# Kernel tuning notes

Measured on AMD Instinct MI355X. Metric: run time of the kernel, lower is better.

The kernel has to match this reference:

```python
import jax, jax.numpy as jnp
import numpy as np


def setup_inputs() -> dict:
    key = jax.random.key(0)
    ks = jax.random.split(key, 7)
    b, t, c = 2, 2048, 1024
    s = 0.02  # keep pre-softmax logits in a sane range
    return {
        "query": jax.random.normal(ks[0], (b, t, c), jnp.float32),
        "key": jax.random.normal(ks[1], (b, t, c), jnp.float32),
        "value": jax.random.normal(ks[2], (b, t, c), jnp.float32),
        "in_proj_w": jax.random.normal(ks[3], (3 * c, c), jnp.float32) * s,
        "in_proj_b": jax.random.normal(ks[4], (3 * c,), jnp.float32) * s,
        "out_proj_w": jax.random.normal(ks[5], (c, c), jnp.float32) * s,
        "out_proj_b": jax.random.normal(ks[6], (c,), jnp.float32) * s,
        "window_size": 128,
    }


def reference(query, key, value, in_proj_w, in_proj_b, out_proj_w, out_proj_b, window_size):
    num_heads = 16
    b, t, c = query.shape
    hd = c // num_heads
    wq, wk, wv = in_proj_w[:c], in_proj_w[c:2 * c], in_proj_w[2 * c:]
    bq, bk, bv = in_proj_b[:c], in_proj_b[c:2 * c], in_proj_b[2 * c:]
    # project and split heads: [b, h, t, hd]
    q = (query @ wq.T + bq).reshape(b, t, num_heads, hd).transpose(0, 2, 1, 3)
    k = (key @ wk.T + bk).reshape(b, t, num_heads, hd).transpose(0, 2, 1, 3)
    v = (value @ wv.T + bv).reshape(b, t, num_heads, hd).transpose(0, 2, 1, 3)
    # NOTE: torch adds a *float* attn_mask to the logits. The original mask is
    # 1.0 inside the sliding window, 0.0 outside -- an additive +1 bias, NOT -inf.
    idx = jnp.arange(t)
    band = (jnp.abs(idx[:, None] - idx[None, :]) <= window_size).astype(q.dtype)  # [t, t]
    scale = 1.0 / jnp.sqrt(jnp.asarray(hd, q.dtype))
    logits = jnp.einsum("bhqd,bhkd->bhqk", q * scale, k) + band  # [b,h,t,t]
    attn = jax.nn.softmax(logits, axis=-1)
    out = jnp.einsum("bhqk,bhkd->bhqd", attn, v)  # [b,h,t,hd]
    out = out.transpose(0, 2, 1, 3).reshape(b, t, c)
    return out @ out_proj_w.T + out_proj_b
```

## Files before the change

### kernel.cpp

```cpp
#include <hip/hip_runtime.h>

typedef __attribute__((ext_vector_type(8)))  short short8;
typedef __attribute__((ext_vector_type(4)))  short sh4;
typedef __attribute__((ext_vector_type(4)))  float f32x4;
typedef __attribute__((ext_vector_type(16))) float f32x16;

constexpr int B  = 2;
constexpr int T  = 2048;
constexpr int C  = 1024;
constexpr int H  = 16;
constexpr int HD = 64;

__device__ inline unsigned bf16rne(float a){
  unsigned u = __builtin_bit_cast(unsigned, a);
  u += 0x7fffu + ((u >> 16) & 1u);
  return u >> 16;
}
__device__ inline unsigned bf16pair(float a, float b){
  unsigned ua = __builtin_bit_cast(unsigned, a); ua += 0x7fffu + ((ua >> 16) & 1u);
  unsigned ub = __builtin_bit_cast(unsigned, b); ub += 0x7fffu + ((ub >> 16) & 1u);
  return (ua >> 16) | (ub & 0xffff0000u);
}
__device__ inline void gll16(const void* g, void* l){
  __builtin_amdgcn_global_load_lds(
      (const __attribute__((address_space(1))) unsigned*)g,
      (__attribute__((address_space(3))) unsigned*)l, 16, 0, 0);
}
__device__ inline float exp2f_(float x){
#if __has_builtin(__builtin_amdgcn_exp2f)
  return __builtin_amdgcn_exp2f(x);
#else
  return __builtin_exp2f(x);
#endif
}

__global__ void convert_k(const float* __restrict__ ipw, const float* __restrict__ opw,
                          const float* __restrict__ q, const float* __restrict__ k,
                          const float* __restrict__ v, unsigned* __restrict__ dst)
{
  const int i = blockIdx.x * 256 + threadIdx.x;
  const long e = (long)i * 4;
  const float* src; long off;
  if      (e <  3145728) { src = ipw; off = e; }
  else if (e <  4194304) { src = opw; off = e - 3145728; }
  else if (e <  8388608) { src = q;   off = e - 4194304; }
  else if (e < 12582912) { src = k;   off = e - 8388608; }
  else                   { src = v;   off = e - 12582912; }
  const float4 x = *(const float4*)(src + off);
  dst[i*2+0] = bf16pair(x.x, x.y);
  dst[i*2+1] = bf16pair(x.z, x.w);
}

template<int MODE>
__global__ __launch_bounds__(256, 2) void gemm_k(
    const unsigned short* __restrict__ A0, const unsigned short* __restrict__ A1,
    const unsigned short* __restrict__ A2,
    const unsigned short* __restrict__ Wb, const float* __restrict__ bias,
    unsigned short* __restrict__ Qb, unsigned short* __restrict__ Kb,
    unsigned short* __restrict__ Vt, float* __restrict__ outF)
{
  __shared__ __align__(16) unsigned short As[128*32];
  __shared__ __align__(16) unsigned short Bs[128*32];
  const int tid  = threadIdx.x, lane = tid & 63, wv = tid >> 6;
  const int wm   = wv & 1, wn = wv >> 1;
  const int bm   = blockIdx.x, bn = blockIdx.y;
  const int m16  = lane & 15, quad = lane >> 4;

  const int which = (MODE == 0) ? (bn >> 3) : 0;
  const unsigned short* A = (which == 0) ? A0 : (which == 1 ? A1 : A2);

  f32x4 acc[4][4];
#pragma unroll
  for (int i = 0; i < 4; i++)
#pragma unroll
    for (int j = 0; j < 4; j++) acc[i][j] = (f32x4){0.f, 0.f, 0.f, 0.f};

  const int srow = wv * 32 + (lane >> 2);
  const int skp  = (lane & 3) * 8;

  for (int k0 = 0; k0 < 1024; k0 += 32) {
    __syncthreads();
#pragma unroll
    for (int p = 0; p < 2; p++) {
      gll16(A  + (size_t)(bm*128 + srow + p*16)*1024 + k0 + skp,
            (char*)As + wv*2048 + p*1024);
      gll16(Wb + (size_t)(bn*128 + srow + p*16)*1024 + k0 + skp,
            (char*)Bs + wv*2048 + p*1024);
    }
    __syncthreads();

    short8 af[4], bf[4];
#pragma unroll
    for (int i = 0; i < 4; i++)
      af[i] = *(const short8*)((const char*)As + (wm*64 + i*16 + m16)*64 + quad*16);
#pragma unroll
    for (int j = 0; j < 4; j++)
      bf[j] = *(const short8*)((const char*)Bs + (wn*64 + j*16 + m16)*64 + quad*16);
#pragma unroll
    for (int i = 0; i < 4; i++)
#pragma unroll
      for (int j = 0; j < 4; j++)
        acc[i][j] = __builtin_amdgcn_mfma_f32_16x16x32_bf16(af[i], bf[j], acc[i][j], 0,0,0);
  }

#pragma unroll
  for (int j = 0; j < 4; j++) {
    const int n_e = bn*128 + wn*64 + j*16 + m16;
    const float bj = bias[n_e];
    const int rem = n_e & 1023;
    const int hh = rem >> 6, dd = rem & 63;
#pragma unroll
    for (int i = 0; i < 4; i++) {
      const int mbase = bm*128 + wm*64 + i*16 + quad*4;
      if constexpr (MODE == 1) {
#pragma unroll
        for (int r = 0; r < 4; r++)
          outF[(size_t)(mbase + r) * 1024 + n_e] = acc[i][j][r] + bj;
      } else {
        const int b = mbase >> 11, tl = mbase & 2047;
        if (which == 2) {
          sh4 pv;
#pragma unroll
          for (int r = 0; r < 4; r++) pv[r] = (short)bf16rne(acc[i][j][r] + bj);
          *(sh4*)(Vt + ((size_t)((b*16 + hh)*64 + dd))*2048 + tl) = pv;
        } else {
          unsigned short* dst = (which == 0 ? Qb : Kb);
#pragma unroll
          for (int r = 0; r < 4; r++)
            dst[(size_t)((b*16 + hh)*2048 + tl + r)*64 + dd] =
                (unsigned short)bf16rne(acc[i][j][r] + bj);
        }
      }
    }
  }
}

__global__ __launch_bounds__(256, 2) void attn_k(
    const unsigned short* __restrict__ Qb, const unsigned short* __restrict__ Kb,
    const unsigned short* __restrict__ Vt, const int* __restrict__ wptr,
    unsigned short* __restrict__ ctx)
{
  __shared__ __align__(16) char smem[16896];
  unsigned short* Kl = (unsigned short*)smem;
  unsigned short* Vl = (unsigned short*)(smem + 8192);
  float* Om   = (float*)smem;
  float* lbuf = (float*)(smem + 16384);

  const int tid = threadIdx.x, lane = tid & 63, wv = tid >> 6;
  const int wq = wv >> 1, wk = wv & 1;
  const int h = lane >> 5, ln = lane & 31;
  const bool hs = (h == 1);
  const int qt = blockIdx.x, bh = blockIdx.y;
  const int win = *wptr;
  const int q0 = qt * 64 + wq * 32;
  const size_t hb = (size_t)bh * T * HD;

  constexpr float LOG2E = 1.44269504f;
  constexpr float C1    = 0.125f * LOG2E;

  short8 qf[4];
#pragma unroll
  for (int s = 0; s < 4; s++)
    qf[s] = *(const short8*)(Qb + hb + (size_t)(q0 + ln)*64 + s*16 + h*8);

  short8 onesv;
#pragma unroll
  for (int jj = 0; jj < 8; jj++) onesv[jj] = (short)0x3F80;

  f32x16 O0, O1, Lacc, Zv;
#pragma unroll
  for (int r = 0; r < 16; r++) { O0[r] = 0.f; O1[r] = 0.f; Lacc[r] = 0.f; Zv[r] = 0.f; }
  const int tq = q0 + ln;

  for (int kt = 0; kt < 32; ++kt) {
    __syncthreads();
#pragma unroll
    for (int p = 0; p < 2; p++) {
      const int c2 = wv*2 + p;
      gll16(Kb + hb + (size_t)(kt*64 + lane)*64 + c2*8, (char*)Kl + c2*1024);
      gll16(Vt + hb + (size_t)lane*T + kt*64 + c2*8,    (char*)Vl + c2*1024);
    }
    __syncthreads();

    f32x16 st;
#pragma unroll
    for (int s = 0; s < 4; s++) {
      const short8 kf = *(const short8*)((const char*)Kl + (2*s + h)*1024 + (wk*32 + ln)*16);
      st = __builtin_amdgcn_mfma_f32_32x32x16_bf16(kf, qf[s], (s == 0 ? Zv : st), 0, 0, 0);
    }

    const int kb = kt*64 + wk*32;
    int sep = 0;
    if (kb > q0 + 31) sep = kb - (q0 + 31);
    else if (q0 > kb + 31) sep = q0 - (kb + 31);
    const int d1 = kb + 31 - q0, d2 = q0 + 31 - kb;
    const int dmax = max(d1 < 0 ? -d1 : d1, d2 < 0 ? -d2 : d2);

    float pr[16];
    if (sep > win) {
#pragma unroll
      for (int r = 0; r < 16; r++) pr[r] = exp2f_(st[r] * C1);
    } else if (dmax <= win) {
#pragma unroll
      for (int r = 0; r < 16; r++) pr[r] = exp2f_(__builtin_fmaf(st[r], C1, LOG2E));
    } else {
      const int tkb = kb + 4*h;
#pragma unroll
      for (int r = 0; r < 16; r++) {
        const int tk = tkb + (r & 3) + 8*(r >> 2);
        int dd = tq - tk; dd = dd < 0 ? -dd : dd;
        pr[r] = exp2f_(__builtin_fmaf(st[r], C1, dd <= win ? LOG2E : 0.0f));
      }
    }

    unsigned pk[8];
#pragma unroll
    for (int g = 0; g < 8; g++)
      pk[g] = __builtin_amdgcn_perm(__builtin_bit_cast(unsigned, pr[2*g+1]),
                                    __builtin_bit_cast(unsigned, pr[2*g]),
                                    0x07060302u);

#pragma unroll
    for (int c = 0; c < 2; c++) {
      const unsigned sh0 = (unsigned)__shfl_xor((int)pk[4*c+0], 32, 64);
      const unsigned sh1 = (unsigned)__shfl_xor((int)pk[4*c+1], 32, 64);
      const unsigned sh2 = (unsigned)__shfl_xor((int)pk[4*c+2], 32, 64);
      const unsigned sh3 = (unsigned)__shfl_xor((int)pk[4*c+3], 32, 64);
      union { unsigned u[4]; short8 v; } P;
      P.u[0] = hs ? sh2 : pk[4*c+0];
      P.u[1] = hs ? sh3 : pk[4*c+1];
      P.u[2] = hs ? pk[4*c+2] : sh0;
      P.u[3] = hs ? pk[4*c+3] : sh1;
#pragma unroll
      for (int dt = 0; dt < 2; dt++) {
        const short8 vf = *(const short8*)((const char*)Vl + (wk*4 + 2*c + h)*1024 + (dt*32 + ln)*16);
        if (dt == 0) O0 = __builtin_amdgcn_mfma_f32_32x32x16_bf16(P.v, vf, O0, 0,0,0);
        else         O1 = __builtin_amdgcn_mfma_f32_32x32x16_bf16(P.v, vf, O1, 0,0,0);
      }
      Lacc = __builtin_amdgcn_mfma_f32_32x32x16_bf16(P.v, onesv, Lacc, 0,0,0);
    }
  }

  __syncthreads();
  if (wk == 1) {
#pragma unroll
    for (int r = 0; r < 16; r++) {
      Om[wq*2048 + r*64 + lane]        = O0[r];
      Om[wq*2048 + (16 + r)*64 + lane] = O1[r];
    }
    if (ln == 0) {
#pragma unroll
      for (int r = 0; r < 16; r++)
        lbuf[wq*32 + (r & 3) + 8*(r >> 2) + 4*h] = Lacc[r];
    }
  }
  __syncthreads();
  if (wk == 0) {
    const int b = bh >> 4, hh = bh & 15;
#pragma unroll
    for (int r = 0; r < 16; r++) {
      const int qrow = (r & 3) + 8*(r >> 2) + 4*h;
      const float lt = Lacc[r] + lbuf[wq*32 + qrow];
      const float linv = 1.0f / lt;
      const int t = q0 + qrow;
      const float o0 = (O0[r] + Om[wq*2048 + r*64 + lane]) * linv;
      const float o1 = (O1[r] + Om[wq*2048 + (16 + r)*64 + lane]) * linv;
      unsigned short* cp = ctx + (size_t)(b*2048 + t)*1024 + hh*64;
      cp[ln]      = (unsigned short)bf16rne(o0);
      cp[32 + ln] = (unsigned short)bf16rne(o1);
    }
  }
}

extern "C" void kernel_launch(void* const* d_in, const int* in_sizes, int n_in,
                              void* d_out, int out_size, void* d_ws, size_t ws_size,
                              hipStream_t stream)
{
  const float* query = (const float*)d_in[0];
  const float* key   = (const float*)d_in[1];
  const float* value = (const float*)d_in[2];
  const float* ipw   = (const float*)d_in[3];
  const float* ipb   = (const float*)d_in[4];
  const float* opw   = (const float*)d_in[5];
  const float* opb   = (const float*)d_in[6];
  const int*   win   = (const int*)d_in[7];

  char* ws = (char*)d_ws;
  unsigned short* Winbf  = (unsigned short*)(ws);
  unsigned short* Woutbf = (unsigned short*)(ws + 6291456);
  unsigned short* Qin    = (unsigned short*)(ws + 8388608);
  unsigned short* Kin    = (unsigned short*)(ws + 16777216);
  unsigned short* Vin    = (unsigned short*)(ws + 25165824);
  unsigned short* Qb     = (unsigned short*)(ws + 33554432);
  unsigned short* Kb     = (unsigned short*)(ws + 41943040);
  unsigned short* Vt     = (unsigned short*)(ws + 50331648);
  unsigned short* ctx    = (unsigned short*)(ws + 58720256);

  convert_k<<<16384, 256, 0, stream>>>(ipw, opw, query, key, value, (unsigned*)ws);

  gemm_k<0><<<dim3(32, 24), 256, 0, stream>>>(
      Qin, Kin, Vin, Winbf, ipb, Qb, Kb, Vt, nullptr);

  attn_k<<<dim3(32, 32), 256, 0, stream>>>(Qb, Kb, Vt, win, ctx);

  gemm_k<1><<<dim3(32, 8), 256, 0, stream>>>(
      ctx, ctx, ctx, Woutbf, opb, nullptr, nullptr, nullptr, (float*)d_out);
}
```

Before: 242.9 us.

## Double-buffer attention K/V tiles, widen GEMM K-step, stage projection stores via LDS

The attention kernel now prefetches the next K/V tile into registers while computing on the current one, with two LDS buffers so only one barrier is needed per iteration. The GEMM K-step grows from 32 to 64, halving the number of barrier pairs. The QKV projection epilogue goes through LDS so that Q/K/Vt are written with 16-byte coalesced stores instead of scattered 2- and 8-byte writes. Grid axes are swapped for block ordering. The cost is more LDS per block (32KB), which may lower occupancy, and extra barriers in the epilogue.

```diff
diff --git a/kernel.cpp b/kernel.cpp
--- a/kernel.cpp
+++ b/kernel.cpp
@@ -1,7 +1,6 @@
 #include <hip/hip_runtime.h>
 
 typedef __attribute__((ext_vector_type(8)))  short short8;
-typedef __attribute__((ext_vector_type(4)))  short sh4;
 typedef __attribute__((ext_vector_type(4)))  float f32x4;
 typedef __attribute__((ext_vector_type(16))) float f32x16;
 
@@ -59,11 +58,13 @@
     unsigned short* __restrict__ Qb, unsigned short* __restrict__ Kb,
     unsigned short* __restrict__ Vt, float* __restrict__ outF)
 {
-  __shared__ __align__(16) unsigned short As[128*32];
-  __shared__ __align__(16) unsigned short Bs[128*32];
+  __shared__ __align__(16) char gsm[32768];
+  unsigned short* As = (unsigned short*)gsm;
+  unsigned short* Bs = (unsigned short*)(gsm + 16384);
+
   const int tid  = threadIdx.x, lane = tid & 63, wv = tid >> 6;
   const int wm   = wv & 1, wn = wv >> 1;
-  const int bm   = blockIdx.x, bn = blockIdx.y;
+  const int bn   = blockIdx.x, bm = blockIdx.y;
   const int m16  = lane & 15, quad = lane >> 4;
 
   const int which = (MODE == 0) ? (bn >> 3) : 0;
@@ -75,61 +76,112 @@
 #pragma unroll
     for (int j = 0; j < 4; j++) acc[i][j] = (f32x4){0.f, 0.f, 0.f, 0.f};
 
-  const int srow = wv * 32 + (lane >> 2);
-  const int skp  = (lane & 3) * 8;
-
-  for (int k0 = 0; k0 < 1024; k0 += 32) {
+  const int srow = (lane >> 3);
+  const int skp  = (lane & 7) * 8;
+
+  for (int k0 = 0; k0 < 1024; k0 += 64) {
     __syncthreads();
 #pragma unroll
-    for (int p = 0; p < 2; p++) {
-      gll16(A  + (size_t)(bm*128 + srow + p*16)*1024 + k0 + skp,
-            (char*)As + wv*2048 + p*1024);
-      gll16(Wb + (size_t)(bn*128 + srow + p*16)*1024 + k0 + skp,
-            (char*)Bs + wv*2048 + p*1024);
+    for (int p = 0; p < 4; p++) {
+      const int row = wv*32 + p*8 + srow;
+      gll16(A  + (size_t)(bm*128 + row)*1024 + k0 + skp, (char*)As + (wv*4+p)*1024);
+      gll16(Wb + (size_t)(bn*128 + row)*1024 + k0 + skp, (char*)Bs + (wv*4+p)*1024);
     }
     __syncthreads();
 
-    short8 af[4], bf[4];
-#pragma unroll
-    for (int i = 0; i < 4; i++)
-      af[i] = *(const short8*)((const char*)As + (wm*64 + i*16 + m16)*64 + quad*16);
-#pragma unroll
-    for (int j = 0; j < 4; j++)
-      bf[j] = *(const short8*)((const char*)Bs + (wn*64 + j*16 + m16)*64 + quad*16);
-#pragma unroll
-    for (int i = 0; i < 4; i++)
+    short8 af[2][4], bf2[2][4];
+#pragma unroll
+    for (int kh = 0; kh < 2; kh++) {
+#pragma unroll
+      for (int i = 0; i < 4; i++)
+        af[kh][i] = *(const short8*)((const char*)As + (wm*64 + i*16 + m16)*128 + kh*64 + quad*16);
 #pragma unroll
       for (int j = 0; j < 4; j++)
-        acc[i][j] = __builtin_amdgcn_mfma_f32_16x16x32_bf16(af[i], bf[j], acc[i][j], 0,0,0);
-  }
-
-#pragma unroll
-  for (int j = 0; j < 4; j++) {
-    const int n_e = bn*128 + wn*64 + j*16 + m16;
-    const float bj = bias[n_e];
-    const int rem = n_e & 1023;
-    const int hh = rem >> 6, dd = rem & 63;
-#pragma unroll
-    for (int i = 0; i < 4; i++) {
-      const int mbase = bm*128 + wm*64 + i*16 + quad*4;
-      if constexpr (MODE == 1) {
+        bf2[kh][j] = *(const short8*)((const char*)Bs + (wn*64 + j*16 + m16)*128 + kh*64 + quad*16);
+    }
+#pragma unroll
+    for (int kh = 0; kh < 2; kh++)
+#pragma unroll
+      for (int i = 0; i < 4; i++)
+#pragma unroll
+        for (int j = 0; j < 4; j++)
+          acc[i][j] = __builtin_amdgcn_mfma_f32_16x16x32_bf16(af[kh][i], bf2[kh][j], acc[i][j], 0,0,0);
+  }
+
+  if constexpr (MODE == 1) {
+#pragma unroll
+    for (int j = 0; j < 4; j++) {
+      const int n_e = bn*128 + wn*64 + j*16 + m16;
+      const float bj = bias[n_e];
+#pragma unroll
+      for (int i = 0; i < 4; i++) {
+        const int mbase = bm*128 + wm*64 + i*16 + quad*4;
 #pragma unroll
         for (int r = 0; r < 4; r++)
           outF[(size_t)(mbase + r) * 1024 + n_e] = acc[i][j][r] + bj;
-      } else {
-        const int b = mbase >> 11, tl = mbase & 2047;
-        if (which == 2) {
-          sh4 pv;
-#pragma unroll
-          for (int r = 0; r < 4; r++) pv[r] = (short)bf16rne(acc[i][j][r] + bj);
-          *(sh4*)(Vt + ((size_t)((b*16 + hh)*64 + dd))*2048 + tl) = pv;
-        } else {
-          unsigned short* dst = (which == 0 ? Qb : Kb);
-#pragma unroll
-          for (int r = 0; r < 4; r++)
-            dst[(size_t)((b*16 + hh)*2048 + tl + r)*64 + dd] =
-                (unsigned short)bf16rne(acc[i][j][r] + bj);
+      }
+    }
+  } else {
+    __syncthreads();
+    float* Ls = (float*)gsm;
+    const int hbase = (bn & 7) * 2;
+    const int b = bm >> 4;
+    const int tbase = (bm & 15) * 128;
+    if (which < 2) {
+      unsigned short* dst = (which == 0 ? Qb : Kb);
+#pragma unroll
+      for (int j = 0; j < 4; ++j) {
+        const float bj = bias[bn*128 + wn*64 + j*16 + m16];
+#pragma unroll
+        for (int i = 0; i < 4; ++i) {
+          const int m0 = wm*64 + i*16 + quad*4;
+#pragma unroll
+          for (int r = 0; r < 4; ++r)
+            Ls[(m0 + r)*36 + wn*16 + m16] = acc[i][j][r] + bj;
         }
+        __syncthreads();
+#pragma unroll
+        for (int r2 = 0; r2 < 2; ++r2) {
+          const int v = r2*256 + tid;
+          const int m = v & 127, seg = v >> 7;
+          const int wn2 = seg >> 1, d0 = j*16 + (seg & 1)*8;
+          const float* src = &Ls[m*36 + wn2*16 + (seg & 1)*8];
+          const float4 f0 = *(const float4*)src;
+          const float4 f1 = *(const float4*)(src + 4);
+          uint4 st;
+          st.x = bf16pair(f0.x, f0.y); st.y = bf16pair(f0.z, f0.w);
+          st.z = bf16pair(f1.x, f1.y); st.w = bf16pair(f1.z, f1.w);
+          *(uint4*)&dst[((size_t)((b*16 + hbase + wn2)*2048 + tbase + m))*64 + d0] = st;
+        }
+        __syncthreads();
+      }
+    } else {
+#pragma unroll
+      for (int j = 0; j < 4; ++j) {
+        const float bj = bias[bn*128 + wn*64 + j*16 + m16];
+        const int col = wn*16 + m16;
+#pragma unroll
+        for (int i = 0; i < 4; ++i) {
+          f32x4 tv = acc[i][j];
+          tv[0] += bj; tv[1] += bj; tv[2] += bj; tv[3] += bj;
+          *(f32x4*)&Ls[col*132 + wm*64 + i*16 + quad*4] = tv;
+        }
+        __syncthreads();
+#pragma unroll
+        for (int r2 = 0; r2 < 2; ++r2) {
+          const int v = r2*256 + tid;
+          const int n = v >> 4, mseg = v & 15;
+          const float* src = &Ls[n*132 + mseg*8];
+          const float4 f0 = *(const float4*)src;
+          const float4 f1 = *(const float4*)(src + 4);
+          uint4 st;
+          st.x = bf16pair(f0.x, f0.y); st.y = bf16pair(f0.z, f0.w);
+          st.z = bf16pair(f1.x, f1.y); st.w = bf16pair(f1.z, f1.w);
+          const int d = j*16 + (n & 15);
+          const int hh = hbase + (n >> 4);
+          *(uint4*)&Vt[(((size_t)(b*16 + hh))*64 + d)*2048 + tbase + mseg*8] = st;
+        }
+        __syncthreads();
       }
     }
   }
@@ -140,17 +192,15 @@
     const unsigned short* __restrict__ Vt, const int* __restrict__ wptr,
     unsigned short* __restrict__ ctx)
 {
-  __shared__ __align__(16) char smem[16896];
-  unsigned short* Kl = (unsigned short*)smem;
-  unsigned short* Vl = (unsigned short*)(smem + 8192);
+  __shared__ __align__(16) char smem[33024];
   float* Om   = (float*)smem;
-  float* lbuf = (float*)(smem + 16384);
+  float* lbuf = (float*)(smem + 32768);
 
   const int tid = threadIdx.x, lane = tid & 63, wv = tid >> 6;
   const int wq = wv >> 1, wk = wv & 1;
   const int h = lane >> 5, ln = lane & 31;
   const bool hs = (h == 1);
-  const int qt = blockIdx.x, bh = blockIdx.y;
+  const int bh = blockIdx.x, qt = blockIdx.y;
   const int win = *wptr;
   const int q0 = qt * 64 + wq * 32;
   const size_t hb = (size_t)bh * T * HD;
@@ -172,20 +222,41 @@
   for (int r = 0; r < 16; r++) { O0[r] = 0.f; O1[r] = 0.f; Lacc[r] = 0.f; Zv[r] = 0.f; }
   const int tq = q0 + ln;
 
+  const int srow = tid >> 2;
+  const int soff = (tid & 3) * 16;
+  const int c0   = (tid & 3) * 2;
+  const unsigned short* Kg = Kb + hb;
+  const unsigned short* Vg = Vt + hb;
+
+  uint4 ka, kb2, va, vb;
+  ka  = *(const uint4*)(Kg + (size_t)srow*64 + soff);
+  kb2 = *(const uint4*)(Kg + (size_t)srow*64 + soff + 8);
+  va  = *(const uint4*)(Vg + (size_t)srow*2048 + soff);
+  vb  = *(const uint4*)(Vg + (size_t)srow*2048 + soff + 8);
+  {
+    char* Kd = smem; char* Vd = smem + 8192;
+    *(uint4*)(Kd + c0*1024 + srow*16)     = ka;
+    *(uint4*)(Kd + (c0+1)*1024 + srow*16) = kb2;
+    *(uint4*)(Vd + c0*1024 + srow*16)     = va;
+    *(uint4*)(Vd + (c0+1)*1024 + srow*16) = vb;
+  }
+  __syncthreads();
+
   for (int kt = 0; kt < 32; ++kt) {
-    __syncthreads();
-#pragma unroll
-    for (int p = 0; p < 2; p++) {
-      const int c2 = wv*2 + p;
-      gll16(Kb + hb + (size_t)(kt*64 + lane)*64 + c2*8, (char*)Kl + c2*1024);
-      gll16(Vt + hb + (size_t)lane*T + kt*64 + c2*8,    (char*)Vl + c2*1024);
-    }
-    __syncthreads();
+    if (kt < 31) {
+      const int t1 = (kt + 1) * 64;
+      ka  = *(const uint4*)(Kg + (size_t)(t1 + srow)*64 + soff);
+      kb2 = *(const uint4*)(Kg + (size_t)(t1 + srow)*64 + soff + 8);
+      va  = *(const uint4*)(Vg + (size_t)srow*2048 + t1 + soff);
+      vb  = *(const uint4*)(Vg + (size_t)srow*2048 + t1 + soff + 8);
+    }
+    const char* Kl = smem + (kt & 1)*16384;
+    const char* Vl = Kl + 8192;
 
     f32x16 st;
 #pragma unroll
     for (int s = 0; s < 4; s++) {
-      const short8 kf = *(const short8*)((const char*)Kl + (2*s + h)*1024 + (wk*32 + ln)*16);
+      const short8 kf = *(const short8*)(Kl + (2*s + h)*1024 + (wk*32 + ln)*16);
       st = __builtin_amdgcn_mfma_f32_32x32x16_bf16(kf, qf[s], (s == 0 ? Zv : st), 0, 0, 0);
     }
 
@@ -233,11 +304,21 @@
       P.u[3] = hs ? pk[4*c+3] : sh1;
 #pragma unroll
       for (int dt = 0; dt < 2; dt++) {
-        const short8 vf = *(const short8*)((const char*)Vl + (wk*4 + 2*c + h)*1024 + (dt*32 + ln)*16);
+        const short8 vf = *(const short8*)(Vl + (wk*4 + 2*c + h)*1024 + (dt*32 + ln)*16);
         if (dt == 0) O0 = __builtin_amdgcn_mfma_f32_32x32x16_bf16(P.v, vf, O0, 0,0,0);
         else         O1 = __builtin_amdgcn_mfma_f32_32x32x16_bf16(P.v, vf, O1, 0,0,0);
       }
       Lacc = __builtin_amdgcn_mfma_f32_32x32x16_bf16(P.v, onesv, Lacc, 0,0,0);
+    }
+
+    if (kt < 31) {
+      char* Kd = smem + ((kt + 1) & 1)*16384;
+      char* Vd = Kd + 8192;
+      *(uint4*)(Kd + c0*1024 + srow*16)     = ka;
+      *(uint4*)(Kd + (c0+1)*1024 + srow*16) = kb2;
+      *(uint4*)(Vd + c0*1024 + srow*16)     = va;
+      *(uint4*)(Vd + (c0+1)*1024 + srow*16) = vb;
+      __syncthreads();
     }
   }
 
@@ -298,11 +379,11 @@
 
   convert_k<<<16384, 256, 0, stream>>>(ipw, opw, query, key, value, (unsigned*)ws);
 
-  gemm_k<0><<<dim3(32, 24), 256, 0, stream>>>(
+  gemm_k<0><<<dim3(24, 32), 256, 0, stream>>>(
       Qin, Kin, Vin, Winbf, ipb, Qb, Kb, Vt, nullptr);
 
   attn_k<<<dim3(32, 32), 256, 0, stream>>>(Qb, Kb, Vt, win, ctx);
 
-  gemm_k<1><<<dim3(32, 8), 256, 0, stream>>>(
+  gemm_k<1><<<dim3(8, 32), 256, 0, stream>>>(
       ctx, ctx, ctx, Woutbf, opb, nullptr, nullptr, nullptr, (float*)d_out);
 }
```

New measurement: 245.1 us. About the same (+0.9%).
